# Performance work log

Hardware: AMD Instinct MI355X
Metric: run time of the kernel (lower is better)

## Reference

```python
import jax, jax.numpy as jnp
import numpy as np

EPS = 1e-10

def _pairwise_cos_dist(X, Y):
    # X: (N, c), Y: (M, c) -> (N, M) cosine distance, matching torch impl exactly
    x_norm = jnp.sqrt(jnp.sum(X * X, axis=1, keepdims=True))          # (N, 1)
    y_norm = jnp.sqrt(jnp.sum(Y * Y, axis=1, keepdims=True)).T        # (1, M)
    return 1.0 - (X @ Y.T) / (x_norm + EPS) / (y_norm + EPS)

def _style_loss_cos(X, Y):
    D = _pairwise_cos_dist(X, Y)
    m1 = jnp.min(D, axis=1).mean()  # relaxed EMD, row mins
    m2 = jnp.min(D, axis=0).mean()  # col mins
    return jnp.maximum(m1, m2)

def _moment_loss(X, Y):
    # X, Y: (N, c)
    n = X.shape[0]
    mu_x = X.mean(axis=0, keepdims=True)
    mu_y = Y.mean(axis=0, keepdims=True)
    mu_d = jnp.abs(mu_x - mu_y).mean()
    Xc = X - mu_x
    Yc = Y - mu_y
    X_cov = (Xc.T @ Xc) / (n - 1)   # (c, c)
    Y_cov = (Yc.T @ Yc) / (n - 1)
    return mu_d + jnp.abs(X_cov - Y_cov).mean()

def _level_loss(X, Y):
    # X, Y: (N, c) per-batch, per-level feature sets
    return _style_loss_cos(X, Y) + _moment_loss(X, Y)

_per_batch_level_loss = jax.vmap(_level_loss)  # over leading batch dim

def _gather_points(feat, idx):
    # feat: (B, c, h, w), idx: (B, N) spatial indices -> (B, N, c)
    B, c, h, w = feat.shape
    flat = feat.reshape(B, c, h * w)
    g = jnp.take_along_axis(flat, idx[:, None, :], axis=2)  # (B, c, N)
    return jnp.swapaxes(g, 1, 2)

def _all_points(feat):
    # feat: (B, c, h, w) -> (B, h*w, c); used when h <= 32 (no subsampling)
    B, c, h, w = feat.shape
    return jnp.swapaxes(feat.reshape(B, c, h * w), 1, 2)

def setup_inputs() -> dict:
    key = jax.random.key(0)
    ks = jax.random.split(key, 11)
    shapes = [(8, 64, 256, 256), (8, 128, 128, 128), (8, 256, 64, 64), (8, 512, 32, 32)]
    inp = {}
    for i, s in enumerate(shapes):
        inp[f"target_feat{i}"] = jax.random.normal(ks[i], s, dtype=jnp.float32)
        inp[f"gen_feat{i}"] = jax.random.normal(ks[4 + i], s, dtype=jnp.float32)
    for j, hw in enumerate([256 * 256, 128 * 128, 64 * 64]):
        inp[f"idx{j}"] = jnp.sort(
            jax.random.randint(ks[8 + j], (8, 1000), 0, hw, dtype=jnp.int32), axis=1
        )
    return inp

def reference(target_feat0, target_feat1, target_feat2, target_feat3,
              gen_feat0, gen_feat1, gen_feat2, gen_feat3,
              idx0, idx1, idx2):
    B = target_feat0.shape[0]
    loss_b = jnp.zeros((B,), dtype=target_feat0.dtype)
    # levels 0-2: h > 32 -> subsample 1000 spatial points
    for t, g, idx in [(target_feat0, gen_feat0, idx0),
                      (target_feat1, gen_feat1, idx1),
                      (target_feat2, gen_feat2, idx2)]:
        loss_b = loss_b + _per_batch_level_loss(_gather_points(t, idx), _gather_points(g, idx))
    # level 3: h == 32 -> use all 1024 points
    loss_b = loss_b + _per_batch_level_loss(_all_points(target_feat3), _all_points(gen_feat3))
    return loss_b.mean()  # sum over batch / batch_size
```

## Files before the change

### kernel.cpp

```cpp
#include <hip/hip_runtime.h>
#include <cstdint>
#include <cstddef>

#define EPSC 1e-10f
typedef unsigned short u16;
typedef unsigned int u32;
typedef __attribute__((ext_vector_type(8))) short bf16x8;
typedef __attribute__((ext_vector_type(4))) float f32x4;

#define XTX_B 0u
#define XTY_B 7864320u
#define XNX_B 15728640u
#define XNY_B 23592960u
#define FB 15728640u
#define RNX_OFF (FB + 0u)
#define RNY_OFF (FB + 32768u)
#define RMIN_OFF (FB + 65536u)
#define CMIN_OFF (FB + 98304u)
#define MUX_OFF (FB + 131072u)
#define MUY_OFF (FB + 138752u)
#define COVS_OFF (FB + 146432u)
#define ACC_OFF (FB + 146464u)

struct Tabs { int c[4], N[4], mo[4]; u32 off[4]; };
struct GArgs {
  const float* t[4];
  const float* g[4];
  const int* idx[4];
  int c[4], hw[4], N[4], mo[4];
  u32 off[4];
};

__device__ __forceinline__ u16 f2bf(float f) {
  u32 u = __float_as_uint(f);
  u = (u + 0x7fffu + ((u >> 16) & 1u)) >> 16;
  return (u16)u;
}
__device__ __forceinline__ float bf2f(u16 h) { return __uint_as_float(((u32)h) << 16); }

__global__ void k_init(float* __restrict__ wsf) {
  int i = blockIdx.x * blockDim.x + threadIdx.x;
  if (i < 65536) ((unsigned*)(wsf + RMIN_OFF))[i] = 0x7f800000u;
  if (i < 65536) wsf[RNX_OFF + i] = 0.f;
  if (i < 15393) wsf[MUX_OFF + i] = 0.f;
}

__global__ void k_gather_all(GArgs ga, u16* __restrict__ bfb, float* __restrict__ wsf) {
  __shared__ float Ls[64 * 67];
  __shared__ float Rs[64];
  int y = blockIdx.y;
  int L = (y >= 7) ? 3 : (y >= 3) ? 2 : (y >= 1) ? 1 : 0;
  int ybase = (L == 0) ? 0 : (L == 1) ? 1 : (L == 2) ? 3 : 7;
  int cb64 = y - ybase;
  int c = ga.c[L], hw = ga.hw[L], N = ga.N[L];
  const int* idx = ga.idx[L];
  int z = blockIdx.z, which = z >> 3, b = z & 7;
  int c0 = cb64 * 64, n0 = blockIdx.x * 64;
  int tid = threadIdx.x;
  const float* src = which ? ga.g[L] : ga.t[L];
  u16* dt = bfb + (which ? XTY_B : XTX_B) + ga.off[L] + (size_t)b * c * 1024;
  u16* dn = bfb + (which ? XNY_B : XNX_B) + ga.off[L] + (size_t)b * c * 1024;
  float* musum = wsf + (which ? MUY_OFF : MUX_OFF) + ga.mo[L] + (size_t)b * c + c0;
  float* rnsum = wsf + (which ? RNY_OFF : RNX_OFF) + (size_t)(L * 8 + b) * 1024 + n0;
  int nl = tid & 63, cb = tid >> 6;
  int n = n0 + nl;
  bool nv = n < N;
  int sp = nv ? (idx ? idx[b * N + n] : n) : 0;
  const float* sbase = src + ((size_t)b * c + c0) * hw;
  float v[16];
#pragma unroll
  for (int r = 0; r < 16; ++r) {
    int ch = cb + r * 4;
    v[r] = nv ? sbase[(size_t)ch * hw + sp] : 0.f;
    Ls[ch * 67 + nl] = v[r];
  }
  if (tid < 64) Rs[tid] = 0.f;
  float s2 = 0.f;
#pragma unroll
  for (int r = 0; r < 16; ++r) s2 = fmaf(v[r], v[r], s2);
#pragma unroll
  for (int r = 0; r < 16; ++r) {
    float s = v[r];
#pragma unroll
    for (int off = 32; off; off >>= 1) s += __shfl_down(s, off, 64);
    if (nl == 0) atomicAdd(&musum[cb + r * 4], s);
  }
  __syncthreads();
  atomicAdd(&Rs[nl], s2);
#pragma unroll
  for (int r = 0; r < 16; ++r) {
    int ch = cb + r * 4;
    dt[(size_t)(c0 + ch) * 1024 + n] = f2bf(Ls[ch * 67 + nl]);
  }
#pragma unroll
  for (int r = 0; r < 16; ++r) {
    int nw = cb + r * 4;
    int chw = nl;
    dn[(size_t)(n0 + nw) * c + c0 + chw] = f2bf(Ls[chw * 67 + nw]);
  }
  __syncthreads();
  if (tid < 64) atomicAdd(&rnsum[tid], Rs[tid]);
}

__global__ __launch_bounds__(256) void k_cosmin(const u16* __restrict__ bfb, float* __restrict__ wsf, Tabs t) {
  int z = blockIdx.z, L = z >> 3, b = z & 7;
  int c = t.c[L], N = t.N[L];
  const u16* X = bfb + XNX_B + t.off[L] + (size_t)b * c * 1024;
  const u16* Y = bfb + XNY_B + t.off[L] + (size_t)b * c * 1024;
  int i0 = blockIdx.x * 128, j0 = blockIdx.y * 128;
  int tid = threadIdx.x, lane = tid & 63, w = tid >> 6;
  int wi = w >> 1, wj = w & 1, q = lane >> 4, cl = lane & 15;
  const u16* ap[4];
  const u16* bp[4];
#pragma unroll
  for (int u = 0; u < 4; ++u) {
    ap[u] = X + (size_t)(i0 + wi * 64 + u * 16 + cl) * c + q * 8;
    bp[u] = Y + (size_t)(j0 + wj * 64 + u * 16 + cl) * c + q * 8;
  }
  f32x4 acc[4][4] = {};
  for (int k0 = 0; k0 < c; k0 += 32) {
    bf16x8 af[4], bq4[4];
#pragma unroll
    for (int u = 0; u < 4; ++u) af[u] = *(const bf16x8*)(ap[u] + k0);
#pragma unroll
    for (int u = 0; u < 4; ++u) bq4[u] = *(const bf16x8*)(bp[u] + k0);
#pragma unroll
    for (int ti = 0; ti < 4; ++ti)
#pragma unroll
      for (int tj = 0; tj < 4; ++tj)
        acc[ti][tj] = __builtin_amdgcn_mfma_f32_16x16x32_bf16(af[ti], bq4[tj], acc[ti][tj], 0, 0, 0);
  }
  const float* rnx = wsf + RNX_OFF + (size_t)z * 1024;
  const float* rny = wsf + RNY_OFF + (size_t)z * 1024;
  unsigned* rminp = (unsigned*)(wsf + RMIN_OFF) + (size_t)z * 1024;
  unsigned* cminp = (unsigned*)(wsf + CMIN_OFF) + (size_t)z * 1024;
  const float INFV = __uint_as_float(0x7f800000u);
  int colg[4]; float rnyv[4]; float colmin[4];
#pragma unroll
  for (int tj = 0; tj < 4; ++tj) {
    colg[tj] = j0 + wj * 64 + tj * 16 + cl;
    rnyv[tj] = 1.0f / (sqrtf(rny[colg[tj]]) + EPSC);
    colmin[tj] = INFV;
  }
#pragma unroll
  for (int ti = 0; ti < 4; ++ti) {
#pragma unroll
    for (int r = 0; r < 4; ++r) {
      int rowg = i0 + wi * 64 + ti * 16 + q * 4 + r;
      float rx = 1.0f / (sqrtf(rnx[rowg]) + EPSC);
      bool rv = rowg < N;
      float rmin = INFV;
#pragma unroll
      for (int tj = 0; tj < 4; ++tj) {
        float d = 1.0f - acc[ti][tj][r] * rx * rnyv[tj];
        if (!rv || colg[tj] >= N) d = INFV;
        rmin = fminf(rmin, d);
        colmin[tj] = fminf(colmin[tj], d);
      }
      rmin = fminf(rmin, __shfl_xor(rmin, 1, 64));
      rmin = fminf(rmin, __shfl_xor(rmin, 2, 64));
      rmin = fminf(rmin, __shfl_xor(rmin, 4, 64));
      rmin = fminf(rmin, __shfl_xor(rmin, 8, 64));
      if (cl == 0 && rv) atomicMin(&rminp[rowg], __float_as_uint(rmin));
    }
  }
#pragma unroll
  for (int tj = 0; tj < 4; ++tj) {
    float cm = colmin[tj];
    cm = fminf(cm, __shfl_xor(cm, 16, 64));
    cm = fminf(cm, __shfl_xor(cm, 32, 64));
    if (q == 0 && colg[tj] < N) atomicMin(&cminp[colg[tj]], __float_as_uint(cm));
  }
}

#define COVW_NBLK 370
__global__ __launch_bounds__(256) void k_covw(const u16* __restrict__ bfb, float* __restrict__ wsf, Tabs t) {
  int bid = blockIdx.x;
  int qx = COVW_NBLK >> 3, rx = COVW_NBLK & 7;
  int xcd = bid & 7, pos = bid >> 3;
  int bsw = (xcd < rx ? xcd * (qx + 1) : rx * (qx + 1) + (xcd - rx) * qx) + pos;
  int w = bsw * 4 + (threadIdx.x >> 6);
  int L, b, tt, W;
  if (w < 1088)      { int r = w;        L = 3; b = r / 136; tt = r - b * 136; W = 16; }
  else if (w < 1376) { int r = w - 1088; L = 2; b = r / 36;  tt = r - b * 36;  W = 8; }
  else if (w < 1456) { int r = w - 1376; L = 1; b = r / 10;  tt = r - b * 10;  W = 4; }
  else               { int r = w - 1456; L = 0; b = r / 3;   tt = r - b * 3;   W = 2; }
  int ti = 0, rem = tt;
  while (rem >= W - ti) { rem -= (W - ti); ++ti; }
  int tj = ti + rem;
  int c = t.c[L], N = t.N[L];
  const u16* Xp = bfb + XTX_B + t.off[L] + (size_t)b * c * 1024;
  const u16* Yp = bfb + XTY_B + t.off[L] + (size_t)b * c * 1024;
  int lane = threadIdx.x & 63, cl = lane & 15, qq = lane >> 4;
  int i0 = ti * 32, j0 = tj * 32;
  size_t aoff[2], boff[2];
#pragma unroll
  for (int u = 0; u < 2; ++u) {
    aoff[u] = (size_t)(i0 + u * 16 + cl) * 1024 + qq * 8;
    boff[u] = (size_t)(j0 + u * 16 + cl) * 1024 + qq * 8;
  }
  f32x4 acc[2][2] = {};
#pragma unroll 2
  for (int k0 = 0; k0 < 1024; k0 += 32) {
    bf16x8 ax[2], bx[2], ay[2], by[2];
#pragma unroll
    for (int u = 0; u < 2; ++u) {
      ax[u] = *(const bf16x8*)(Xp + aoff[u] + k0);
      bx[u] = *(const bf16x8*)(Xp + boff[u] + k0);
      ay[u] = *(const bf16x8*)(Yp + aoff[u] + k0);
      by[u] = *(const bf16x8*)(Yp + boff[u] + k0);
    }
#pragma unroll
    for (int u = 0; u < 2; ++u) {
      uint4 t4 = *(uint4*)&ay[u];
      t4.x ^= 0x80008000u; t4.y ^= 0x80008000u; t4.z ^= 0x80008000u; t4.w ^= 0x80008000u;
      ay[u] = *(bf16x8*)&t4;
    }
#pragma unroll
    for (int u = 0; u < 2; ++u)
#pragma unroll
      for (int v = 0; v < 2; ++v) {
        acc[u][v] = __builtin_amdgcn_mfma_f32_16x16x32_bf16(ax[u], bx[v], acc[u][v], 0, 0, 0);
        acc[u][v] = __builtin_amdgcn_mfma_f32_16x16x32_bf16(ay[u], by[v], acc[u][v], 0, 0, 0);
      }
  }
  const float* mux = wsf + MUX_OFF + t.mo[L] + (size_t)b * c;
  const float* muy = wsf + MUY_OFF + t.mo[L] + (size_t)b * c;
  float fN = (float)N, inv1 = 1.0f / (float)(N - 1), invN = 1.0f / fN;
  float mxj[2], myj[2];
#pragma unroll
  for (int v = 0; v < 2; ++v) {
    int jg = j0 + v * 16 + cl;
    mxj[v] = mux[jg]; myj[v] = muy[jg];
  }
  float s = 0.f;
#pragma unroll
  for (int u = 0; u < 2; ++u)
#pragma unroll
    for (int r = 0; r < 4; ++r) {
      int ig = i0 + u * 16 + qq * 4 + r;
      float mxi = mux[ig], myi = muy[ig];
#pragma unroll
      for (int v = 0; v < 2; ++v) {
        float d = (acc[u][v][r] - (mxi * mxj[v] - myi * myj[v]) * invN) * inv1;
        s += fabsf(d);
      }
    }
  if (ti != tj) s += s;
#pragma unroll
  for (int o = 1; o < 64; o <<= 1) s += __shfl_xor(s, o, 64);
  if (lane == 0) atomicAdd(&wsf[COVS_OFF + (L * 8 + b)], s);
}

__global__ void k_final(float* __restrict__ wsf, Tabs t) {
  __shared__ float red[4];
  int z = blockIdx.x, L = z >> 3, b = z & 7;
  int c = t.c[L], N = t.N[L];
  const unsigned* rmin = (const unsigned*)(wsf + RMIN_OFF) + (size_t)z * 1024;
  const unsigned* cmin = (const unsigned*)(wsf + CMIN_OFF) + (size_t)z * 1024;
  const float* mux = wsf + MUX_OFF + t.mo[L] + (size_t)b * c;
  const float* muy = wsf + MUY_OFF + t.mo[L] + (size_t)b * c;
  int tid = threadIdx.x;
  float sr = 0.f, sc = 0.f, sm = 0.f;
  for (int n = tid; n < N; n += 256) {
    sr += __uint_as_float(rmin[n]);
    sc += __uint_as_float(cmin[n]);
  }
  for (int ch = tid; ch < c; ch += 256) sm += fabsf(mux[ch] - muy[ch]);
  float vals[3] = {sr, sc, sm};
  float tot[3] = {0.f, 0.f, 0.f};
  for (int qq = 0; qq < 3; ++qq) {
    float v = vals[qq];
#pragma unroll
    for (int off = 32; off; off >>= 1) v += __shfl_down(v, off, 64);
    if ((tid & 63) == 0) red[tid >> 6] = v;
    __syncthreads();
    if (tid == 0) tot[qq] = red[0] + red[1] + red[2] + red[3];
    __syncthreads();
  }
  if (tid == 0) {
    float style = fmaxf(tot[0] / (float)N, tot[1] / (float)N);
    float mu_d = tot[2] / ((float)N * (float)c);
    float cov = wsf[COVS_OFF + z] / ((float)c * (float)c);
    atomicAdd(&wsf[ACC_OFF], style + mu_d + cov);
  }
}

__global__ void k_out(const float* __restrict__ wsf, float* __restrict__ out) {
  if (threadIdx.x == 0 && blockIdx.x == 0) out[0] = wsf[ACC_OFF] * 0.125f;
}

extern "C" void kernel_launch(void* const* d_in, const int* in_sizes, int n_in,
                              void* d_out, int out_size, void* d_ws, size_t ws_size,
                              hipStream_t stream) {
  (void)in_sizes; (void)n_in; (void)out_size; (void)ws_size;
  static const int LC[4] = {64, 128, 256, 512};
  static const int LN[4] = {1000, 1000, 1000, 1024};
  static const int LHW[4] = {65536, 16384, 4096, 1024};
  static const u32 LOFF[4] = {0u, 524288u, 1572864u, 3670016u};
  static const int MO[4] = {0, 512, 1536, 3584};

  float* wsf = (float*)d_ws;
  u16* bfb = (u16*)d_ws;
  Tabs t;
  GArgs ga;
  for (int L = 0; L < 4; ++L) {
    t.c[L] = LC[L]; t.N[L] = LN[L]; t.mo[L] = MO[L]; t.off[L] = LOFF[L];
    ga.t[L] = (const float*)d_in[2 * L];
    ga.g[L] = (const float*)d_in[2 * L + 1];
    ga.idx[L] = (L < 3) ? (const int*)d_in[8 + L] : nullptr;
    ga.c[L] = LC[L]; ga.hw[L] = LHW[L]; ga.N[L] = LN[L]; ga.mo[L] = MO[L]; ga.off[L] = LOFF[L];
  }

  k_init<<<dim3(256), dim3(256), 0, stream>>>(wsf);
  k_gather_all<<<dim3(16, 15, 16), dim3(256), 0, stream>>>(ga, bfb, wsf);
  k_cosmin<<<dim3(8, 8, 32), dim3(256), 0, stream>>>(bfb, wsf, t);
  k_covw<<<dim3(COVW_NBLK), dim3(256), 0, stream>>>(bfb, wsf, t);
  k_final<<<dim3(32), dim3(256), 0, stream>>>(wsf, t);
  k_out<<<dim3(1), dim3(64), 0, stream>>>(wsf, (float*)d_out);
}
```

Baseline: 575.4 us.

## Fuse cosmin and covariance kernels, use direct global-to-LDS gather, fold output write

The gather kernel now loads the strided feature values straight into LDS with global_load_lds and computes the sums from LDS, replacing the per-thread register loads. The cosine-min and covariance MFMA kernels are merged into a single launch, with covariance blocks dispatched first, so the two can overlap and one launch is saved. The final reduction writes the output itself using a completion counter, which removes the separate output kernel. The counter adds an extra atomic and a fence, and the LDS gather now waits on all loads before any arithmetic starts.

```diff
diff --git a/kernel.cpp b/kernel.cpp
--- a/kernel.cpp
+++ b/kernel.cpp
@@ -21,6 +21,7 @@
 #define MUY_OFF (FB + 138752u)
 #define COVS_OFF (FB + 146432u)
 #define ACC_OFF (FB + 146464u)
+#define CNT_OFF (FB + 146465u)
 
 struct Tabs { int c[4], N[4], mo[4]; u32 off[4]; };
 struct GArgs {
@@ -38,11 +39,17 @@
 }
 __device__ __forceinline__ float bf2f(u16 h) { return __uint_as_float(((u32)h) << 16); }
 
+typedef __attribute__((address_space(3))) unsigned lds_as_t;
+typedef __attribute__((address_space(1))) const unsigned glb_as_t;
+__device__ __forceinline__ void gload_lds4(const float* g, float* l) {
+  __builtin_amdgcn_global_load_lds((glb_as_t*)g, (lds_as_t*)l, 4, 0, 0);
+}
+
 __global__ void k_init(float* __restrict__ wsf) {
   int i = blockIdx.x * blockDim.x + threadIdx.x;
   if (i < 65536) ((unsigned*)(wsf + RMIN_OFF))[i] = 0x7f800000u;
   if (i < 65536) wsf[RNX_OFF + i] = 0.f;
-  if (i < 15393) wsf[MUX_OFF + i] = 0.f;
+  if (i < 15394) wsf[MUX_OFF + i] = 0.f;
 }
 
 __global__ void k_gather_all(GArgs ga, u16* __restrict__ bfb, float* __restrict__ wsf) {
@@ -67,47 +74,45 @@
   bool nv = n < N;
   int sp = nv ? (idx ? idx[b * N + n] : n) : 0;
   const float* sbase = src + ((size_t)b * c + c0) * hw;
-  float v[16];
+  if (tid < 64) Rs[tid] = 0.f;
 #pragma unroll
   for (int r = 0; r < 16; ++r) {
     int ch = cb + r * 4;
-    v[r] = nv ? sbase[(size_t)ch * hw + sp] : 0.f;
-    Ls[ch * 67 + nl] = v[r];
-  }
-  if (tid < 64) Rs[tid] = 0.f;
+    gload_lds4(sbase + (size_t)ch * hw + sp, &Ls[ch * 67]);
+  }
+  asm volatile("s_waitcnt vmcnt(0)" ::: "memory");
+  __syncthreads();
   float s2 = 0.f;
-#pragma unroll
-  for (int r = 0; r < 16; ++r) s2 = fmaf(v[r], v[r], s2);
-#pragma unroll
-  for (int r = 0; r < 16; ++r) {
-    float s = v[r];
-#pragma unroll
-    for (int off = 32; off; off >>= 1) s += __shfl_down(s, off, 64);
-    if (nl == 0) atomicAdd(&musum[cb + r * 4], s);
-  }
-  __syncthreads();
-  atomicAdd(&Rs[nl], s2);
 #pragma unroll
   for (int r = 0; r < 16; ++r) {
     int ch = cb + r * 4;
-    dt[(size_t)(c0 + ch) * 1024 + n] = f2bf(Ls[ch * 67 + nl]);
-  }
+    float val = nv ? Ls[ch * 67 + nl] : 0.f;
+    dt[(size_t)(c0 + ch) * 1024 + n] = f2bf(val);
+    s2 = fmaf(val, val, s2);
+    float s = val;
+#pragma unroll
+    for (int off = 32; off; off >>= 1) s += __shfl_down(s, off, 64);
+    if (nl == 0) atomicAdd(&musum[ch], s);
+  }
+  atomicAdd(&Rs[nl], s2);
 #pragma unroll
   for (int r = 0; r < 16; ++r) {
     int nw = cb + r * 4;
-    int chw = nl;
-    dn[(size_t)(n0 + nw) * c + c0 + chw] = f2bf(Ls[chw * 67 + nw]);
+    int ng = n0 + nw;
+    float val = (ng < N) ? Ls[nl * 67 + nw] : 0.f;
+    dn[(size_t)ng * c + c0 + nl] = f2bf(val);
   }
   __syncthreads();
   if (tid < 64) atomicAdd(&rnsum[tid], Rs[tid]);
 }
 
-__global__ __launch_bounds__(256) void k_cosmin(const u16* __restrict__ bfb, float* __restrict__ wsf, Tabs t) {
-  int z = blockIdx.z, L = z >> 3, b = z & 7;
+__device__ __forceinline__ void cosmin_body(const u16* __restrict__ bfb, float* __restrict__ wsf,
+                                            const Tabs& t, int bx, int by, int z) {
+  int L = z >> 3, b = z & 7;
   int c = t.c[L], N = t.N[L];
   const u16* X = bfb + XNX_B + t.off[L] + (size_t)b * c * 1024;
   const u16* Y = bfb + XNY_B + t.off[L] + (size_t)b * c * 1024;
-  int i0 = blockIdx.x * 128, j0 = blockIdx.y * 128;
+  int i0 = bx * 128, j0 = by * 128;
   int tid = threadIdx.x, lane = tid & 63, w = tid >> 6;
   int wi = w >> 1, wj = w & 1, q = lane >> 4, cl = lane & 15;
   const u16* ap[4];
@@ -174,8 +179,8 @@
 }
 
 #define COVW_NBLK 370
-__global__ __launch_bounds__(256) void k_covw(const u16* __restrict__ bfb, float* __restrict__ wsf, Tabs t) {
-  int bid = blockIdx.x;
+__device__ __forceinline__ void covw_body(const u16* __restrict__ bfb, float* __restrict__ wsf,
+                                          const Tabs& t, int bid) {
   int qx = COVW_NBLK >> 3, rx = COVW_NBLK & 7;
   int xcd = bid & 7, pos = bid >> 3;
   int bsw = (xcd < rx ? xcd * (qx + 1) : rx * (qx + 1) + (xcd - rx) * qx) + pos;
@@ -252,7 +257,16 @@
   if (lane == 0) atomicAdd(&wsf[COVS_OFF + (L * 8 + b)], s);
 }
 
-__global__ void k_final(float* __restrict__ wsf, Tabs t) {
+#define FUSE_NBLK (COVW_NBLK + 2048)
+__global__ __launch_bounds__(256) void k_mfma(const u16* __restrict__ bfb, float* __restrict__ wsf, Tabs t) {
+  int bid = blockIdx.x;
+  if (bid < COVW_NBLK) { covw_body(bfb, wsf, t, bid); return; }
+  int cbid = bid - COVW_NBLK;
+  int z = cbid >> 6, rest = cbid & 63;
+  cosmin_body(bfb, wsf, t, rest >> 3, rest & 7, z);
+}
+
+__global__ void k_final(float* __restrict__ wsf, float* __restrict__ out, Tabs t) {
   __shared__ float red[4];
   int z = blockIdx.x, L = z >> 3, b = z & 7;
   int c = t.c[L], N = t.N[L];
@@ -283,11 +297,13 @@
     float mu_d = tot[2] / ((float)N * (float)c);
     float cov = wsf[COVS_OFF + z] / ((float)c * (float)c);
     atomicAdd(&wsf[ACC_OFF], style + mu_d + cov);
-  }
-}
-
-__global__ void k_out(const float* __restrict__ wsf, float* __restrict__ out) {
-  if (threadIdx.x == 0 && blockIdx.x == 0) out[0] = wsf[ACC_OFF] * 0.125f;
+    __threadfence();
+    unsigned old = atomicAdd((unsigned*)&wsf[CNT_OFF], 1u);
+    if (old == 31u) {
+      float acc = atomicAdd(&wsf[ACC_OFF], 0.0f);
+      out[0] = acc * 0.125f;
+    }
+  }
 }
 
 extern "C" void kernel_launch(void* const* d_in, const int* in_sizes, int n_in,
@@ -314,8 +330,6 @@
 
   k_init<<<dim3(256), dim3(256), 0, stream>>>(wsf);
   k_gather_all<<<dim3(16, 15, 16), dim3(256), 0, stream>>>(ga, bfb, wsf);
-  k_cosmin<<<dim3(8, 8, 32), dim3(256), 0, stream>>>(bfb, wsf, t);
-  k_covw<<<dim3(COVW_NBLK), dim3(256), 0, stream>>>(bfb, wsf, t);
-  k_final<<<dim3(32), dim3(256), 0, stream>>>(wsf, t);
-  k_out<<<dim3(1), dim3(64), 0, stream>>>(wsf, (float*)d_out);
-}
+  k_mfma<<<dim3(FUSE_NBLK), dim3(256), 0, stream>>>(bfb, wsf, t);
+  k_final<<<dim3(32), dim3(256), 0, stream>>>(wsf, (float*)d_out, t);
+}
```

Measured after the change: 564.7 us. Within noise of the previous version (-1.9%).
